# Kernel tuning notes

Measured on AMD Instinct MI355X. Metric: run time of the kernel, lower is better.

Reference implementation:

```python
import jax, jax.numpy as jnp
import numpy as np

NUM_CLUSTERS = 64
DIM = 512
ALPHA = 100.0
EPS = 1e-12  # torch F.normalize eps


def setup_inputs() -> dict:
    key = jax.random.key(0)
    k1, k2 = jax.random.split(key)
    x1 = jax.random.normal(k1, (30, DIM, 28, 28), dtype=jnp.float32)
    centroids = jax.random.uniform(k2, (NUM_CLUSTERS, DIM), dtype=jnp.float32)
    # _init_params: conv weight = 2*alpha*centroids (1x1 conv), bias = -alpha*||centroid||
    conv_w = 2.0 * ALPHA * centroids
    conv_b = -ALPHA * jnp.linalg.norm(centroids, axis=1)
    return {"x1": x1, "centroids": centroids, "conv_w": conv_w, "conv_b": conv_b}


def _l2norm(v, axis):
    n = jnp.sqrt(jnp.sum(v * v, axis=axis, keepdims=True))
    return v / jnp.maximum(n, EPS)


def reference(x1, centroids, conv_w, conv_b):
    T, C, H, W = x1.shape
    K, D = centroids.shape
    x = x1.reshape(T, C, H * W)            # [T, C, N]
    x = _l2norm(x, axis=1)                 # normalize_input: L2 over channel dim
    # 1x1 conv == matmul over channels: logits [T, K, N]
    logits = jnp.einsum('kc,tcn->tkn', conv_w, x) + conv_b[None, :, None]
    a = jax.nn.softmax(logits, axis=1)     # soft assignment over clusters
    # vlad[t,k,c] = sum_n a[t,k,n]*(x[t,c,n] - centroids[k,c])
    # rewritten as two small matmuls, avoiding the [K,C,N] residual tensor
    vlad = jnp.einsum('tkn,tcn->tkc', a, x) - a.sum(axis=-1)[:, :, None] * centroids[None]
    vlad = _l2norm(vlad, axis=2)           # intra-normalization over feature dim
    v = vlad.reshape(T, K * D)
    v = _l2norm(v, axis=1)                 # global L2 normalization
    return v.sum(axis=0, keepdims=True)    # [1, K*D] accumulated over 30 timesteps
```

## Files before the change

kernel.cpp:

```cpp
#include <hip/hip_runtime.h>
#include <math.h>

#define T_ 30
#define C_ 512
#define N_ 784
#define NP_ 832
#define EPSV 1e-12f

typedef __attribute__((ext_vector_type(8))) short bf16x8;
typedef __attribute__((ext_vector_type(4))) float f32x4;

__device__ __forceinline__ unsigned short f2bf(float f) {
    union { float f; unsigned int u; } v; v.f = f;
    unsigned int r = (v.u + 0x7FFFu + ((v.u >> 16) & 1u)) >> 16;
    return (unsigned short)r;
}
__device__ __forceinline__ float bf2f(unsigned short h) {
    union { unsigned int u; float f; } v; v.u = ((unsigned int)h) << 16;
    return v.f;
}

__global__ void k_prep(const float* __restrict__ w, unsigned short* __restrict__ wh,
                       unsigned short* __restrict__ wl) {
    int idx = blockIdx.x * 256 + threadIdx.x;
    float v = w[idx];
    unsigned short h = f2bf(v);
    wh[idx] = h;
    wl[idx] = f2bf(v - bf2f(h));
}

__global__ __launch_bounds__(256) void k_assign(
    const float* __restrict__ x, const unsigned short* __restrict__ wh,
    const unsigned short* __restrict__ wl, const float* __restrict__ b,
    unsigned short* __restrict__ aT, float* __restrict__ asum)
{
    __shared__ __align__(16) unsigned short xhT[64 * 130];
    __shared__ __align__(16) unsigned short xlT[64 * 130];
    __shared__ float bloc[64], invl[64], asl[64], ssred[4][64];

    int t = blockIdx.y, n0 = blockIdx.x * 64;
    int tid = threadIdx.x;
    int w = tid >> 6, L = tid & 63, lid = L & 15, quad = L >> 4;

    if (tid < 64) { bloc[tid] = b[tid]; asl[tid] = 0.f; }

    int li = tid & 15;
    int crg = tid >> 4;
    int nbase = n0 + li * 4;
    float ss0 = 0.f, ss1 = 0.f, ss2 = 0.f, ss3 = 0.f;

    f32x4 acc[4];
    #pragma unroll
    for (int mt = 0; mt < 4; ++mt)
        #pragma unroll
        for (int r = 0; r < 4; ++r) acc[mt][r] = 0.f;

    for (int ch = 0; ch < 4; ++ch) {
        int c0 = ch * 128;
        #pragma unroll
        for (int p = 0; p < 8; ++p) {
            int cl = p * 16 + crg;
            const float* xp = x + ((size_t)t * C_ + c0 + cl) * N_ + nbase;
            float v0, v1, v2, v3;
            if (nbase + 3 < N_) {
                float4 q = *reinterpret_cast<const float4*>(xp);
                v0 = q.x; v1 = q.y; v2 = q.z; v3 = q.w;
            } else {
                v0 = (nbase + 0 < N_) ? xp[0] : 0.f;
                v1 = (nbase + 1 < N_) ? xp[1] : 0.f;
                v2 = (nbase + 2 < N_) ? xp[2] : 0.f;
                v3 = (nbase + 3 < N_) ? xp[3] : 0.f;
            }
            ss0 = fmaf(v0, v0, ss0); ss1 = fmaf(v1, v1, ss1);
            ss2 = fmaf(v2, v2, ss2); ss3 = fmaf(v3, v3, ss3);
            float vv[4] = {v0, v1, v2, v3};
            #pragma unroll
            for (int j = 0; j < 4; ++j) {
                unsigned short h = f2bf(vv[j]);
                xhT[(li * 4 + j) * 130 + cl] = h;
                xlT[(li * 4 + j) * 130 + cl] = f2bf(vv[j] - bf2f(h));
            }
        }
        __syncthreads();
        #pragma unroll
        for (int ks = 0; ks < 4; ++ks) {
            int cl = ks * 32 + quad * 8;
            bf16x8 bh = *reinterpret_cast<const bf16x8*>(&xhT[(w * 16 + lid) * 130 + cl]);
            bf16x8 blo = *reinterpret_cast<const bf16x8*>(&xlT[(w * 16 + lid) * 130 + cl]);
            int cg = c0 + cl;
            #pragma unroll
            for (int mt = 0; mt < 4; ++mt) {
                bf16x8 ah = *reinterpret_cast<const bf16x8*>(wh + (mt * 16 + lid) * 512 + cg);
                bf16x8 al = *reinterpret_cast<const bf16x8*>(wl + (mt * 16 + lid) * 512 + cg);
                acc[mt] = __builtin_amdgcn_mfma_f32_16x16x32_bf16(ah, bh, acc[mt], 0, 0, 0);
                acc[mt] = __builtin_amdgcn_mfma_f32_16x16x32_bf16(ah, blo, acc[mt], 0, 0, 0);
                acc[mt] = __builtin_amdgcn_mfma_f32_16x16x32_bf16(al, bh, acc[mt], 0, 0, 0);
            }
        }
        __syncthreads();
    }

    ss0 += __shfl_xor(ss0, 16, 64); ss0 += __shfl_xor(ss0, 32, 64);
    ss1 += __shfl_xor(ss1, 16, 64); ss1 += __shfl_xor(ss1, 32, 64);
    ss2 += __shfl_xor(ss2, 16, 64); ss2 += __shfl_xor(ss2, 32, 64);
    ss3 += __shfl_xor(ss3, 16, 64); ss3 += __shfl_xor(ss3, 32, 64);
    if (quad == 0) {
        ssred[w][li * 4 + 0] = ss0; ssred[w][li * 4 + 1] = ss1;
        ssred[w][li * 4 + 2] = ss2; ssred[w][li * 4 + 3] = ss3;
    }
    __syncthreads();
    if (tid < 64) {
        float s = ssred[0][tid] + ssred[1][tid] + ssred[2][tid] + ssred[3][tid];
        invl[tid] = 1.0f / fmaxf(sqrtf(s), EPSV);
    }
    __syncthreads();

    int n_lane = n0 + w * 16 + lid;
    bool valid = n_lane < N_;
    float inv = valid ? invl[w * 16 + lid] : 0.f;
    float lg[16];
    float mx = -1e30f;
    #pragma unroll
    for (int mt = 0; mt < 4; ++mt)
        #pragma unroll
        for (int r = 0; r < 4; ++r) {
            float v = fmaf(acc[mt][r], inv, bloc[mt * 16 + quad * 4 + r]);
            lg[mt * 4 + r] = v;
            mx = fmaxf(mx, v);
        }
    mx = fmaxf(mx, __shfl_xor(mx, 16, 64));
    mx = fmaxf(mx, __shfl_xor(mx, 32, 64));
    float se = 0.f;
    #pragma unroll
    for (int u = 0; u < 16; ++u) { lg[u] = __expf(lg[u] - mx); se += lg[u]; }
    se += __shfl_xor(se, 16, 64);
    se += __shfl_xor(se, 32, 64);
    float rs = 1.0f / se;

    size_t base = (size_t)t * 64 * NP_ + n_lane;
    #pragma unroll
    for (int mt = 0; mt < 4; ++mt)
        #pragma unroll
        for (int r = 0; r < 4; ++r) {
            int k = mt * 16 + quad * 4 + r;
            float a = lg[mt * 4 + r] * rs;
            aT[base + (size_t)k * NP_] = valid ? f2bf(a * inv) : (unsigned short)0;
            float ak = valid ? a : 0.f;
            ak += __shfl_xor(ak, 1, 64); ak += __shfl_xor(ak, 2, 64);
            ak += __shfl_xor(ak, 4, 64); ak += __shfl_xor(ak, 8, 64);
            if (lid == 0) atomicAdd(&asl[k], ak);
        }
    __syncthreads();
    if (tid < 64) atomicAdd(&asum[t * 64 + tid], asl[tid]);
}

__global__ __launch_bounds__(256) void k_vlad(
    const float* __restrict__ x, const unsigned short* __restrict__ aT,
    const float* __restrict__ asum, const float* __restrict__ cent,
    float* __restrict__ vlad)
{
    int t = blockIdx.y, cb = blockIdx.x;
    int tid = threadIdx.x;
    int w = tid >> 6, L = tid & 63, lid = L & 15, quad = L >> 4;
    int c = cb * 64 + w * 16 + lid;

    f32x4 acc[4];
    #pragma unroll
    for (int mt = 0; mt < 4; ++mt)
        #pragma unroll
        for (int r = 0; r < 4; ++r) acc[mt][r] = 0.f;

    const float* xrow = x + ((size_t)t * C_ + c) * N_;
    const unsigned short* ab = aT + (size_t)t * 64 * NP_;

    for (int s = 0; s < 25; ++s) {
        int nb0 = s * 32;
        int nb = nb0 + quad * 8;
        if (nb > N_ - 8) nb = N_ - 8;
        float4 x0 = *reinterpret_cast<const float4*>(xrow + nb);
        float4 x1 = *reinterpret_cast<const float4*>(xrow + nb + 4);
        bf16x8 bb;
        bb[0] = (short)f2bf(x0.x); bb[1] = (short)f2bf(x0.y);
        bb[2] = (short)f2bf(x0.z); bb[3] = (short)f2bf(x0.w);
        bb[4] = (short)f2bf(x1.x); bb[5] = (short)f2bf(x1.y);
        bb[6] = (short)f2bf(x1.z); bb[7] = (short)f2bf(x1.w);
        #pragma unroll
        for (int mt = 0; mt < 4; ++mt) {
            bf16x8 af = *reinterpret_cast<const bf16x8*>(
                ab + (size_t)(mt * 16 + lid) * NP_ + nb0 + quad * 8);
            acc[mt] = __builtin_amdgcn_mfma_f32_16x16x32_bf16(af, bb, acc[mt], 0, 0, 0);
        }
    }
    #pragma unroll
    for (int mt = 0; mt < 4; ++mt)
        #pragma unroll
        for (int r = 0; r < 4; ++r) {
            int k = mt * 16 + quad * 4 + r;
            float v = acc[mt][r] - asum[t * 64 + k] * cent[k * 512 + c];
            vlad[((size_t)t * 64 + k) * 512 + c] = v;
        }
}

__global__ void k_intra(const float* __restrict__ vlad, float* __restrict__ inv_intra,
                        float* __restrict__ g) {
    int w = blockIdx.x * 4 + (threadIdx.x >> 6);
    int lane = threadIdx.x & 63;
    const float* vp = vlad + (size_t)w * 512 + lane;
    float s = 0.f;
    #pragma unroll
    for (int j = 0; j < 8; ++j) { float v = vp[j * 64]; s = fmaf(v, v, s); }
    #pragma unroll
    for (int m = 32; m >= 1; m >>= 1) s += __shfl_xor(s, m, 64);
    float inv = 1.0f / fmaxf(sqrtf(s), EPSV);
    if (lane == 0) { inv_intra[w] = inv; g[w] = s * inv * inv; }
}

__global__ void k_global(const float* __restrict__ g, float* __restrict__ inv_g) {
    int t = threadIdx.x;
    if (t < T_) {
        float s = 0.f;
        for (int k = 0; k < 64; ++k) s += g[t * 64 + k];
        inv_g[t] = 1.0f / fmaxf(sqrtf(s), EPSV);
    }
}

__global__ void k_out(const float* __restrict__ vlad, const float* __restrict__ inv_intra,
                      const float* __restrict__ inv_g, float* __restrict__ out) {
    int idx = blockIdx.x * 256 + threadIdx.x;
    int k = idx >> 9;
    float s = 0.f;
    #pragma unroll 5
    for (int t = 0; t < T_; ++t)
        s += vlad[(size_t)t * 32768 + idx] * inv_intra[t * 64 + k] * inv_g[t];
    out[idx] = s;
}

extern "C" void kernel_launch(void* const* d_in, const int* in_sizes, int n_in,
                              void* d_out, int out_size, void* d_ws, size_t ws_size,
                              hipStream_t stream) {
    const float* x    = (const float*)d_in[0];
    const float* cent = (const float*)d_in[1];
    const float* w    = (const float*)d_in[2];
    const float* b    = (const float*)d_in[3];
    float* out = (float*)d_out;

    float* ws = (float*)d_ws;
    unsigned short* wh = (unsigned short*)ws;
    unsigned short* wl = wh + 32768;
    float* asum = (float*)(wl + 32768);
    unsigned short* aT = (unsigned short*)(asum + 1920);
    float* vlad = (float*)(aT + (size_t)T_ * 64 * NP_);
    float* inv_intra = vlad + 983040;
    float* g         = inv_intra + 1920;
    float* inv_g     = g + 1920;

    k_prep<<<128, 256, 0, stream>>>(w, wh, wl);
    hipMemsetAsync(asum, 0, 1920 * sizeof(float), stream);
    k_assign<<<dim3(13, T_), 256, 0, stream>>>(x, wh, wl, b, aT, asum);
    k_vlad<<<dim3(8, T_), 256, 0, stream>>>(x, aT, asum, cent, vlad);
    k_intra<<<480, 256, 0, stream>>>(vlad, inv_intra, g);
    k_global<<<1, 64, 0, stream>>>(g, inv_g);
    k_out<<<128, 256, 0, stream>>>(vlad, inv_intra, inv_g, out);
}
```

Measured before the change: 161.1 us.

## Add transpose/precast pass and split assign/vlad into single-wave blocks

Adds a k_trans kernel that reads x once, computes per-pixel sum of squares via atomics, and writes bf16 hi/lo copies in [n,c] layout plus a bf16 [c,n] copy for the vlad stage. k_assign and k_vlad then run as 64-thread single-wave blocks over many more blocks, reading the pre-cast bf16 data directly instead of converting fp32 inside through LDS. k_global is folded into k_out. The aim is better parallelism and less conversion work. The cost is an extra pass writing about three bf16 copies of x and extra memsets.

After: 176.8 us. 9.8% more time.

```diff
diff --git a/kernel.cpp b/kernel.cpp
--- a/kernel.cpp
+++ b/kernel.cpp
@@ -5,6 +5,7 @@
 #define C_ 512
 #define N_ 784
 #define NP_ 832
+#define NB_ 800
 #define EPSV 1e-12f
 
 typedef __attribute__((ext_vector_type(8))) short bf16x8;
@@ -29,25 +30,86 @@
     wl[idx] = f2bf(v - bf2f(h));
 }
 
-__global__ __launch_bounds__(256) void k_assign(
-    const float* __restrict__ x, const unsigned short* __restrict__ wh,
-    const unsigned short* __restrict__ wl, const float* __restrict__ b,
+__global__ __launch_bounds__(256) void k_trans(
+    const float* __restrict__ x, unsigned short* __restrict__ xh,
+    unsigned short* __restrict__ xl, unsigned short* __restrict__ xcn,
+    float* __restrict__ sumsq)
+{
+    __shared__ float sx[64][65];
+    __shared__ float wred[4][64];
+    int nt = blockIdx.x, ct = blockIdx.y, t = blockIdx.z;
+    int n0 = nt * 64, c0 = ct * 64;
+    int tid = threadIdx.x;
+    int cr = tid >> 4, li = tid & 15;
+    int w = tid >> 6;
+    float ss[4] = {0.f, 0.f, 0.f, 0.f};
+
+    #pragma unroll
+    for (int j = 0; j < 4; ++j) {
+        int cl = j * 16 + cr;
+        int n = n0 + li * 4;
+        float4 q = make_float4(0.f, 0.f, 0.f, 0.f);
+        if (n < N_)
+            q = *reinterpret_cast<const float4*>(x + ((size_t)t * C_ + c0 + cl) * N_ + n);
+        ss[0] = fmaf(q.x, q.x, ss[0]); ss[1] = fmaf(q.y, q.y, ss[1]);
+        ss[2] = fmaf(q.z, q.z, ss[2]); ss[3] = fmaf(q.w, q.w, ss[3]);
+        sx[cl][li * 4 + 0] = q.x; sx[cl][li * 4 + 1] = q.y;
+        sx[cl][li * 4 + 2] = q.z; sx[cl][li * 4 + 3] = q.w;
+    }
+    #pragma unroll
+    for (int i = 0; i < 4; ++i) {
+        ss[i] += __shfl_xor(ss[i], 16, 64);
+        ss[i] += __shfl_xor(ss[i], 32, 64);
+    }
+    if (((tid >> 4) & 3) == 0) {
+        wred[w][li * 4 + 0] = ss[0]; wred[w][li * 4 + 1] = ss[1];
+        wred[w][li * 4 + 2] = ss[2]; wred[w][li * 4 + 3] = ss[3];
+    }
+    __syncthreads();
+    if (tid < 64 && n0 + tid < N_) {
+        float s = wred[0][tid] + wred[1][tid] + wred[2][tid] + wred[3][tid];
+        atomicAdd(&sumsq[t * N_ + n0 + tid], s);
+    }
+    {
+        int li2 = tid & 15, nr = tid >> 4;
+        #pragma unroll
+        for (int j = 0; j < 4; ++j) {
+            int nl = nr + j * 16;
+            ushort4 h, l;
+            float v0 = sx[li2 * 4 + 0][nl], v1 = sx[li2 * 4 + 1][nl];
+            float v2 = sx[li2 * 4 + 2][nl], v3 = sx[li2 * 4 + 3][nl];
+            h.x = f2bf(v0); l.x = f2bf(v0 - bf2f(h.x));
+            h.y = f2bf(v1); l.y = f2bf(v1 - bf2f(h.y));
+            h.z = f2bf(v2); l.z = f2bf(v2 - bf2f(h.z));
+            h.w = f2bf(v3); l.w = f2bf(v3 - bf2f(h.w));
+            size_t o = ((size_t)t * NP_ + n0 + nl) * C_ + c0 + li2 * 4;
+            *reinterpret_cast<ushort4*>(xh + o) = h;
+            *reinterpret_cast<ushort4*>(xl + o) = l;
+        }
+    }
+    #pragma unroll
+    for (int j = 0; j < 4; ++j) {
+        int cl = j * 16 + cr;
+        int n = n0 + li * 4;
+        if (n < NB_) {
+            ushort4 h;
+            h.x = f2bf(sx[cl][li * 4 + 0]); h.y = f2bf(sx[cl][li * 4 + 1]);
+            h.z = f2bf(sx[cl][li * 4 + 2]); h.w = f2bf(sx[cl][li * 4 + 3]);
+            *reinterpret_cast<ushort4*>(xcn + ((size_t)t * C_ + c0 + cl) * NB_ + n) = h;
+        }
+    }
+}
+
+__global__ __launch_bounds__(64) void k_assign(
+    const unsigned short* __restrict__ xh, const unsigned short* __restrict__ xl,
+    const unsigned short* __restrict__ wh, const unsigned short* __restrict__ wl,
+    const float* __restrict__ b, const float* __restrict__ sumsq,
     unsigned short* __restrict__ aT, float* __restrict__ asum)
 {
-    __shared__ __align__(16) unsigned short xhT[64 * 130];
-    __shared__ __align__(16) unsigned short xlT[64 * 130];
-    __shared__ float bloc[64], invl[64], asl[64], ssred[4][64];
-
-    int t = blockIdx.y, n0 = blockIdx.x * 64;
-    int tid = threadIdx.x;
-    int w = tid >> 6, L = tid & 63, lid = L & 15, quad = L >> 4;
-
-    if (tid < 64) { bloc[tid] = b[tid]; asl[tid] = 0.f; }
-
-    int li = tid & 15;
-    int crg = tid >> 4;
-    int nbase = n0 + li * 4;
-    float ss0 = 0.f, ss1 = 0.f, ss2 = 0.f, ss3 = 0.f;
+    int t = blockIdx.y;
+    int n0 = blockIdx.x * 16;
+    int L = threadIdx.x & 63, lid = L & 15, quad = L >> 4;
+    int n_lane = n0 + lid;
 
     f32x4 acc[4];
     #pragma unroll
@@ -55,76 +117,43 @@
         #pragma unroll
         for (int r = 0; r < 4; ++r) acc[mt][r] = 0.f;
 
-    for (int ch = 0; ch < 4; ++ch) {
-        int c0 = ch * 128;
-        #pragma unroll
-        for (int p = 0; p < 8; ++p) {
-            int cl = p * 16 + crg;
-            const float* xp = x + ((size_t)t * C_ + c0 + cl) * N_ + nbase;
-            float v0, v1, v2, v3;
-            if (nbase + 3 < N_) {
-                float4 q = *reinterpret_cast<const float4*>(xp);
-                v0 = q.x; v1 = q.y; v2 = q.z; v3 = q.w;
-            } else {
-                v0 = (nbase + 0 < N_) ? xp[0] : 0.f;
-                v1 = (nbase + 1 < N_) ? xp[1] : 0.f;
-                v2 = (nbase + 2 < N_) ? xp[2] : 0.f;
-                v3 = (nbase + 3 < N_) ? xp[3] : 0.f;
-            }
-            ss0 = fmaf(v0, v0, ss0); ss1 = fmaf(v1, v1, ss1);
-            ss2 = fmaf(v2, v2, ss2); ss3 = fmaf(v3, v3, ss3);
-            float vv[4] = {v0, v1, v2, v3};
-            #pragma unroll
-            for (int j = 0; j < 4; ++j) {
-                unsigned short h = f2bf(vv[j]);
-                xhT[(li * 4 + j) * 130 + cl] = h;
-                xlT[(li * 4 + j) * 130 + cl] = f2bf(vv[j] - bf2f(h));
-            }
-        }
-        __syncthreads();
-        #pragma unroll
-        for (int ks = 0; ks < 4; ++ks) {
-            int cl = ks * 32 + quad * 8;
-            bf16x8 bh = *reinterpret_cast<const bf16x8*>(&xhT[(w * 16 + lid) * 130 + cl]);
-            bf16x8 blo = *reinterpret_cast<const bf16x8*>(&xlT[(w * 16 + lid) * 130 + cl]);
-            int cg = c0 + cl;
-            #pragma unroll
-            for (int mt = 0; mt < 4; ++mt) {
-                bf16x8 ah = *reinterpret_cast<const bf16x8*>(wh + (mt * 16 + lid) * 512 + cg);
-                bf16x8 al = *reinterpret_cast<const bf16x8*>(wl + (mt * 16 + lid) * 512 + cg);
-                acc[mt] = __builtin_amdgcn_mfma_f32_16x16x32_bf16(ah, bh, acc[mt], 0, 0, 0);
-                acc[mt] = __builtin_amdgcn_mfma_f32_16x16x32_bf16(ah, blo, acc[mt], 0, 0, 0);
-                acc[mt] = __builtin_amdgcn_mfma_f32_16x16x32_bf16(al, bh, acc[mt], 0, 0, 0);
-            }
-        }
-        __syncthreads();
-    }
-
-    ss0 += __shfl_xor(ss0, 16, 64); ss0 += __shfl_xor(ss0, 32, 64);
-    ss1 += __shfl_xor(ss1, 16, 64); ss1 += __shfl_xor(ss1, 32, 64);
-    ss2 += __shfl_xor(ss2, 16, 64); ss2 += __shfl_xor(ss2, 32, 64);
-    ss3 += __shfl_xor(ss3, 16, 64); ss3 += __shfl_xor(ss3, 32, 64);
-    if (quad == 0) {
-        ssred[w][li * 4 + 0] = ss0; ssred[w][li * 4 + 1] = ss1;
-        ssred[w][li * 4 + 2] = ss2; ssred[w][li * 4 + 3] = ss3;
-    }
-    __syncthreads();
-    if (tid < 64) {
-        float s = ssred[0][tid] + ssred[1][tid] + ssred[2][tid] + ssred[3][tid];
-        invl[tid] = 1.0f / fmaxf(sqrtf(s), EPSV);
-    }
-    __syncthreads();
-
-    int n_lane = n0 + w * 16 + lid;
+    const unsigned short* bp = xh + ((size_t)t * NP_ + n_lane) * C_ + quad * 8;
+    const unsigned short* blp = xl + ((size_t)t * NP_ + n_lane) * C_ + quad * 8;
+
+    #pragma unroll 4
+    for (int ks = 0; ks < 16; ++ks) {
+        int cs = ks * 32;
+        bf16x8 bh = *reinterpret_cast<const bf16x8*>(bp + cs);
+        bf16x8 bl = *reinterpret_cast<const bf16x8*>(blp + cs);
+        #pragma unroll
+        for (int mt = 0; mt < 4; ++mt) {
+            const unsigned short* ar = wh + (size_t)(mt * 16 + lid) * C_ + cs + quad * 8;
+            const unsigned short* alr = wl + (size_t)(mt * 16 + lid) * C_ + cs + quad * 8;
+            bf16x8 ah = *reinterpret_cast<const bf16x8*>(ar);
+            bf16x8 al = *reinterpret_cast<const bf16x8*>(alr);
+            acc[mt] = __builtin_amdgcn_mfma_f32_16x16x32_bf16(ah, bh, acc[mt], 0, 0, 0);
+            acc[mt] = __builtin_amdgcn_mfma_f32_16x16x32_bf16(al, bh, acc[mt], 0, 0, 0);
+            acc[mt] = __builtin_amdgcn_mfma_f32_16x16x32_bf16(ah, bl, acc[mt], 0, 0, 0);
+        }
+    }
+
     bool valid = n_lane < N_;
-    float inv = valid ? invl[w * 16 + lid] : 0.f;
+    float inv = 0.f;
+    if (valid) {
+        float s = sumsq[t * N_ + n_lane];
+        inv = 1.0f / fmaxf(sqrtf(s), EPSV);
+    }
+    f32x4 bv[4];
+    #pragma unroll
+    for (int mt = 0; mt < 4; ++mt)
+        bv[mt] = *reinterpret_cast<const f32x4*>(b + mt * 16 + quad * 4);
     float lg[16];
     float mx = -1e30f;
     #pragma unroll
     for (int mt = 0; mt < 4; ++mt)
         #pragma unroll
         for (int r = 0; r < 4; ++r) {
-            float v = fmaf(acc[mt][r], inv, bloc[mt * 16 + quad * 4 + r]);
+            float v = fmaf(acc[mt][r], inv, bv[mt][r]);
             lg[mt * 4 + r] = v;
             mx = fmaxf(mx, v);
         }
@@ -137,32 +166,29 @@
     se += __shfl_xor(se, 32, 64);
     float rs = 1.0f / se;
 
-    size_t base = (size_t)t * 64 * NP_ + n_lane;
+    size_t abase = (size_t)t * 64 * NP_ + n_lane;
     #pragma unroll
     for (int mt = 0; mt < 4; ++mt)
         #pragma unroll
         for (int r = 0; r < 4; ++r) {
             int k = mt * 16 + quad * 4 + r;
             float a = lg[mt * 4 + r] * rs;
-            aT[base + (size_t)k * NP_] = valid ? f2bf(a * inv) : (unsigned short)0;
+            aT[abase + (size_t)k * NP_] = valid ? f2bf(a * inv) : (unsigned short)0;
             float ak = valid ? a : 0.f;
             ak += __shfl_xor(ak, 1, 64); ak += __shfl_xor(ak, 2, 64);
             ak += __shfl_xor(ak, 4, 64); ak += __shfl_xor(ak, 8, 64);
-            if (lid == 0) atomicAdd(&asl[k], ak);
-        }
-    __syncthreads();
-    if (tid < 64) atomicAdd(&asum[t * 64 + tid], asl[tid]);
-}
-
-__global__ __launch_bounds__(256) void k_vlad(
-    const float* __restrict__ x, const unsigned short* __restrict__ aT,
+            if (lid == 0) atomicAdd(&asum[t * 64 + k], ak);
+        }
+}
+
+__global__ __launch_bounds__(64) void k_vlad(
+    const unsigned short* __restrict__ xcn, const unsigned short* __restrict__ aT,
     const float* __restrict__ asum, const float* __restrict__ cent,
     float* __restrict__ vlad)
 {
-    int t = blockIdx.y, cb = blockIdx.x;
-    int tid = threadIdx.x;
-    int w = tid >> 6, L = tid & 63, lid = L & 15, quad = L >> 4;
-    int c = cb * 64 + w * 16 + lid;
+    int t = blockIdx.y;
+    int L = threadIdx.x & 63, lid = L & 15, quad = L >> 4;
+    int c = blockIdx.x * 16 + lid;
 
     f32x4 acc[4];
     #pragma unroll
@@ -170,24 +196,16 @@
         #pragma unroll
         for (int r = 0; r < 4; ++r) acc[mt][r] = 0.f;
 
-    const float* xrow = x + ((size_t)t * C_ + c) * N_;
-    const unsigned short* ab = aT + (size_t)t * 64 * NP_;
-
+    const unsigned short* xr = xcn + ((size_t)t * C_ + c) * NB_ + quad * 8;
+    const unsigned short* ab = aT + (size_t)t * 64 * NP_ + quad * 8;
+
+    #pragma unroll 5
     for (int s = 0; s < 25; ++s) {
-        int nb0 = s * 32;
-        int nb = nb0 + quad * 8;
-        if (nb > N_ - 8) nb = N_ - 8;
-        float4 x0 = *reinterpret_cast<const float4*>(xrow + nb);
-        float4 x1 = *reinterpret_cast<const float4*>(xrow + nb + 4);
-        bf16x8 bb;
-        bb[0] = (short)f2bf(x0.x); bb[1] = (short)f2bf(x0.y);
-        bb[2] = (short)f2bf(x0.z); bb[3] = (short)f2bf(x0.w);
-        bb[4] = (short)f2bf(x1.x); bb[5] = (short)f2bf(x1.y);
-        bb[6] = (short)f2bf(x1.z); bb[7] = (short)f2bf(x1.w);
+        int nb = s * 32;
+        bf16x8 bb = *reinterpret_cast<const bf16x8*>(xr + nb);
         #pragma unroll
         for (int mt = 0; mt < 4; ++mt) {
-            bf16x8 af = *reinterpret_cast<const bf16x8*>(
-                ab + (size_t)(mt * 16 + lid) * NP_ + nb0 + quad * 8);
+            bf16x8 af = *reinterpret_cast<const bf16x8*>(ab + (size_t)(mt * 16 + lid) * NP_ + nb);
             acc[mt] = __builtin_amdgcn_mfma_f32_16x16x32_bf16(af, bb, acc[mt], 0, 0, 0);
         }
     }
@@ -215,23 +233,23 @@
     if (lane == 0) { inv_intra[w] = inv; g[w] = s * inv * inv; }
 }
 
-__global__ void k_global(const float* __restrict__ g, float* __restrict__ inv_g) {
-    int t = threadIdx.x;
-    if (t < T_) {
+__global__ void k_out(const float* __restrict__ vlad, const float* __restrict__ inv_intra,
+                      const float* __restrict__ g, float* __restrict__ out) {
+    __shared__ float sinv[T_];
+    int tid = threadIdx.x;
+    if (tid < T_) {
         float s = 0.f;
-        for (int k = 0; k < 64; ++k) s += g[t * 64 + k];
-        inv_g[t] = 1.0f / fmaxf(sqrtf(s), EPSV);
-    }
-}
-
-__global__ void k_out(const float* __restrict__ vlad, const float* __restrict__ inv_intra,
-                      const float* __restrict__ inv_g, float* __restrict__ out) {
-    int idx = blockIdx.x * 256 + threadIdx.x;
+        #pragma unroll 8
+        for (int k = 0; k < 64; ++k) s += g[tid * 64 + k];
+        sinv[tid] = 1.0f / fmaxf(sqrtf(s), EPSV);
+    }
+    __syncthreads();
+    int idx = blockIdx.x * 256 + tid;
     int k = idx >> 9;
     float s = 0.f;
     #pragma unroll 5
     for (int t = 0; t < T_; ++t)
-        s += vlad[(size_t)t * 32768 + idx] * inv_intra[t * 64 + k] * inv_g[t];
+        s += vlad[(size_t)t * 32768 + idx] * inv_intra[t * 64 + k] * sinv[t];
     out[idx] = s;
 }
 
@@ -244,21 +262,25 @@
     const float* b    = (const float*)d_in[3];
     float* out = (float*)d_out;
 
-    float* ws = (float*)d_ws;
-    unsigned short* wh = (unsigned short*)ws;
-    unsigned short* wl = wh + 32768;
-    float* asum = (float*)(wl + 32768);
-    unsigned short* aT = (unsigned short*)(asum + 1920);
-    float* vlad = (float*)(aT + (size_t)T_ * 64 * NP_);
-    float* inv_intra = vlad + 983040;
-    float* g         = inv_intra + 1920;
-    float* inv_g     = g + 1920;
+    char* p = (char*)d_ws;
+    unsigned short* wh = (unsigned short*)p;  p += 65536;
+    unsigned short* wl = (unsigned short*)p;  p += 65536;
+    float* sumsq = (float*)p;                 p += 30 * 784 * 4;
+    float* asum  = (float*)p;                 p += 1920 * 4;
+    unsigned short* aT = (unsigned short*)p;  p += (size_t)30 * 64 * NP_ * 2;
+    unsigned short* xh = (unsigned short*)p;  p += (size_t)30 * NP_ * C_ * 2;
+    unsigned short* xl = (unsigned short*)p;  p += (size_t)30 * NP_ * C_ * 2;
+    unsigned short* xcn = (unsigned short*)p; p += (size_t)30 * C_ * NB_ * 2;
+    float* vlad = (float*)p;                  p += (size_t)983040 * 4;
+    float* inv_intra = (float*)p;             p += 7680;
+    float* g = (float*)p;                     p += 7680;
 
     k_prep<<<128, 256, 0, stream>>>(w, wh, wl);
-    hipMemsetAsync(asum, 0, 1920 * sizeof(float), stream);
-    k_assign<<<dim3(13, T_), 256, 0, stream>>>(x, wh, wl, b, aT, asum);
-    k_vlad<<<dim3(8, T_), 256, 0, stream>>>(x, aT, asum, cent, vlad);
+    hipMemsetAsync(sumsq, 0, 30 * 784 * 4, stream);
+    hipMemsetAsync(asum, 0, 1920 * 4, stream);
+    k_trans<<<dim3(13, 8, T_), 256, 0, stream>>>(x, xh, xl, xcn, sumsq);
+    k_assign<<<dim3(52, T_), 64, 0, stream>>>(xh, xl, wh, wl, b, sumsq, aT, asum);
+    k_vlad<<<dim3(32, T_), 64, 0, stream>>>(xcn, aT, asum, cent, vlad);
     k_intra<<<480, 256, 0, stream>>>(vlad, inv_intra, g);
-    k_global<<<1, 64, 0, stream>>>(g, inv_g);
-    k_out<<<128, 256, 0, stream>>>(vlad, inv_intra, inv_g, out);
-}
+    k_out<<<128, 256, 0, stream>>>(vlad, inv_intra, g, out);
+}
```

## Split channel reduction across waves, raise grid size, fuse norm kernels

Applied to the files above, without the earlier changes.

k_assign now uses 16-pixel tiles (49x30 blocks) with the channel dimension split across the four waves and reduced through LDS. k_vlad uses 16-channel tiles (32x30 blocks) with the pixel dimension split across waves, and it also accumulates squared norms by atomic adds. This removes the separate k_intra and k_global kernels, which are folded into k_out. The aim is higher occupancy on a GPU with many CUs and fewer launches, at the cost of an extra LDS reduction, more atomics, and an added memset of aT.

New measurement: 150.9 us. -6.4%, faster.

```diff
diff --git a/kernel.cpp b/kernel.cpp
--- a/kernel.cpp
+++ b/kernel.cpp
@@ -4,7 +4,8 @@
 #define T_ 30
 #define C_ 512
 #define N_ 784
-#define NP_ 832
+#define NA_ 800
+#define XPITCH 520
 #define EPSV 1e-12f
 
 typedef __attribute__((ext_vector_type(8))) short bf16x8;
@@ -34,20 +35,49 @@
     const unsigned short* __restrict__ wl, const float* __restrict__ b,
     unsigned short* __restrict__ aT, float* __restrict__ asum)
 {
-    __shared__ __align__(16) unsigned short xhT[64 * 130];
-    __shared__ __align__(16) unsigned short xlT[64 * 130];
-    __shared__ float bloc[64], invl[64], asl[64], ssred[4][64];
-
-    int t = blockIdx.y, n0 = blockIdx.x * 64;
+    __shared__ __align__(16) char smem[2 * 16 * XPITCH * 2];
+    unsigned short* xh = (unsigned short*)smem;
+    unsigned short* xl = xh + 16 * XPITCH;
+    float* red = (float*)smem;
+    __shared__ float ssq[4][16];
+    __shared__ float invl[16];
+
+    int t = blockIdx.y, n0 = blockIdx.x * 16;
     int tid = threadIdx.x;
     int w = tid >> 6, L = tid & 63, lid = L & 15, quad = L >> 4;
 
-    if (tid < 64) { bloc[tid] = b[tid]; asl[tid] = 0.f; }
-
-    int li = tid & 15;
-    int crg = tid >> 4;
-    int nbase = n0 + li * 4;
+    int nseg = (tid & 3) * 4;
+    int crow = tid >> 2;
     float ss0 = 0.f, ss1 = 0.f, ss2 = 0.f, ss3 = 0.f;
+    #pragma unroll
+    for (int p = 0; p < 8; ++p) {
+        int c = p * 64 + crow;
+        float4 q = *reinterpret_cast<const float4*>(
+            x + ((size_t)t * C_ + c) * N_ + n0 + nseg);
+        ss0 = fmaf(q.x, q.x, ss0); ss1 = fmaf(q.y, q.y, ss1);
+        ss2 = fmaf(q.z, q.z, ss2); ss3 = fmaf(q.w, q.w, ss3);
+        float vv[4] = {q.x, q.y, q.z, q.w};
+        #pragma unroll
+        for (int j = 0; j < 4; ++j) {
+            unsigned short h = f2bf(vv[j]);
+            xh[(nseg + j) * XPITCH + c] = h;
+            xl[(nseg + j) * XPITCH + c] = f2bf(vv[j] - bf2f(h));
+        }
+    }
+    #pragma unroll
+    for (int m = 4; m <= 32; m <<= 1) {
+        ss0 += __shfl_xor(ss0, m, 64); ss1 += __shfl_xor(ss1, m, 64);
+        ss2 += __shfl_xor(ss2, m, 64); ss3 += __shfl_xor(ss3, m, 64);
+    }
+    if (L < 4) {
+        ssq[w][L * 4 + 0] = ss0; ssq[w][L * 4 + 1] = ss1;
+        ssq[w][L * 4 + 2] = ss2; ssq[w][L * 4 + 3] = ss3;
+    }
+    __syncthreads();
+    if (tid < 16) {
+        float s = ssq[0][tid] + ssq[1][tid] + ssq[2][tid] + ssq[3][tid];
+        invl[tid] = 1.0f / fmaxf(sqrtf(s), EPSV);
+    }
 
     f32x4 acc[4];
     #pragma unroll
@@ -55,114 +85,64 @@
         #pragma unroll
         for (int r = 0; r < 4; ++r) acc[mt][r] = 0.f;
 
-    for (int ch = 0; ch < 4; ++ch) {
-        int c0 = ch * 128;
-        #pragma unroll
-        for (int p = 0; p < 8; ++p) {
-            int cl = p * 16 + crg;
-            const float* xp = x + ((size_t)t * C_ + c0 + cl) * N_ + nbase;
-            float v0, v1, v2, v3;
-            if (nbase + 3 < N_) {
-                float4 q = *reinterpret_cast<const float4*>(xp);
-                v0 = q.x; v1 = q.y; v2 = q.z; v3 = q.w;
-            } else {
-                v0 = (nbase + 0 < N_) ? xp[0] : 0.f;
-                v1 = (nbase + 1 < N_) ? xp[1] : 0.f;
-                v2 = (nbase + 2 < N_) ? xp[2] : 0.f;
-                v3 = (nbase + 3 < N_) ? xp[3] : 0.f;
-            }
-            ss0 = fmaf(v0, v0, ss0); ss1 = fmaf(v1, v1, ss1);
-            ss2 = fmaf(v2, v2, ss2); ss3 = fmaf(v3, v3, ss3);
-            float vv[4] = {v0, v1, v2, v3};
-            #pragma unroll
-            for (int j = 0; j < 4; ++j) {
-                unsigned short h = f2bf(vv[j]);
-                xhT[(li * 4 + j) * 130 + cl] = h;
-                xlT[(li * 4 + j) * 130 + cl] = f2bf(vv[j] - bf2f(h));
-            }
-        }
-        __syncthreads();
-        #pragma unroll
-        for (int ks = 0; ks < 4; ++ks) {
-            int cl = ks * 32 + quad * 8;
-            bf16x8 bh = *reinterpret_cast<const bf16x8*>(&xhT[(w * 16 + lid) * 130 + cl]);
-            bf16x8 blo = *reinterpret_cast<const bf16x8*>(&xlT[(w * 16 + lid) * 130 + cl]);
-            int cg = c0 + cl;
-            #pragma unroll
-            for (int mt = 0; mt < 4; ++mt) {
-                bf16x8 ah = *reinterpret_cast<const bf16x8*>(wh + (mt * 16 + lid) * 512 + cg);
-                bf16x8 al = *reinterpret_cast<const bf16x8*>(wl + (mt * 16 + lid) * 512 + cg);
-                acc[mt] = __builtin_amdgcn_mfma_f32_16x16x32_bf16(ah, bh, acc[mt], 0, 0, 0);
-                acc[mt] = __builtin_amdgcn_mfma_f32_16x16x32_bf16(ah, blo, acc[mt], 0, 0, 0);
-                acc[mt] = __builtin_amdgcn_mfma_f32_16x16x32_bf16(al, bh, acc[mt], 0, 0, 0);
-            }
-        }
-        __syncthreads();
-    }
-
-    ss0 += __shfl_xor(ss0, 16, 64); ss0 += __shfl_xor(ss0, 32, 64);
-    ss1 += __shfl_xor(ss1, 16, 64); ss1 += __shfl_xor(ss1, 32, 64);
-    ss2 += __shfl_xor(ss2, 16, 64); ss2 += __shfl_xor(ss2, 32, 64);
-    ss3 += __shfl_xor(ss3, 16, 64); ss3 += __shfl_xor(ss3, 32, 64);
-    if (quad == 0) {
-        ssred[w][li * 4 + 0] = ss0; ssred[w][li * 4 + 1] = ss1;
-        ssred[w][li * 4 + 2] = ss2; ssred[w][li * 4 + 3] = ss3;
-    }
-    __syncthreads();
-    if (tid < 64) {
-        float s = ssred[0][tid] + ssred[1][tid] + ssred[2][tid] + ssred[3][tid];
-        invl[tid] = 1.0f / fmaxf(sqrtf(s), EPSV);
-    }
-    __syncthreads();
-
-    int n_lane = n0 + w * 16 + lid;
-    bool valid = n_lane < N_;
-    float inv = valid ? invl[w * 16 + lid] : 0.f;
-    float lg[16];
-    float mx = -1e30f;
-    #pragma unroll
-    for (int mt = 0; mt < 4; ++mt)
-        #pragma unroll
-        for (int r = 0; r < 4; ++r) {
-            float v = fmaf(acc[mt][r], inv, bloc[mt * 16 + quad * 4 + r]);
-            lg[mt * 4 + r] = v;
-            mx = fmaxf(mx, v);
-        }
-    mx = fmaxf(mx, __shfl_xor(mx, 16, 64));
-    mx = fmaxf(mx, __shfl_xor(mx, 32, 64));
-    float se = 0.f;
-    #pragma unroll
-    for (int u = 0; u < 16; ++u) { lg[u] = __expf(lg[u] - mx); se += lg[u]; }
-    se += __shfl_xor(se, 16, 64);
-    se += __shfl_xor(se, 32, 64);
-    float rs = 1.0f / se;
-
-    size_t base = (size_t)t * 64 * NP_ + n_lane;
-    #pragma unroll
-    for (int mt = 0; mt < 4; ++mt)
-        #pragma unroll
-        for (int r = 0; r < 4; ++r) {
-            int k = mt * 16 + quad * 4 + r;
-            float a = lg[mt * 4 + r] * rs;
-            aT[base + (size_t)k * NP_] = valid ? f2bf(a * inv) : (unsigned short)0;
-            float ak = valid ? a : 0.f;
-            ak += __shfl_xor(ak, 1, 64); ak += __shfl_xor(ak, 2, 64);
-            ak += __shfl_xor(ak, 4, 64); ak += __shfl_xor(ak, 8, 64);
-            if (lid == 0) atomicAdd(&asl[k], ak);
-        }
-    __syncthreads();
-    if (tid < 64) atomicAdd(&asum[t * 64 + tid], asl[tid]);
+    #pragma unroll
+    for (int ks = 0; ks < 4; ++ks) {
+        int cs = w * 128 + ks * 32;
+        bf16x8 bh = *reinterpret_cast<const bf16x8*>(&xh[lid * XPITCH + cs + quad * 8]);
+        bf16x8 bl = *reinterpret_cast<const bf16x8*>(&xl[lid * XPITCH + cs + quad * 8]);
+        #pragma unroll
+        for (int mt = 0; mt < 4; ++mt) {
+            bf16x8 ah = *reinterpret_cast<const bf16x8*>(wh + (size_t)(mt * 16 + lid) * C_ + cs + quad * 8);
+            bf16x8 al = *reinterpret_cast<const bf16x8*>(wl + (size_t)(mt * 16 + lid) * C_ + cs + quad * 8);
+            acc[mt] = __builtin_amdgcn_mfma_f32_16x16x32_bf16(ah, bh, acc[mt], 0, 0, 0);
+            acc[mt] = __builtin_amdgcn_mfma_f32_16x16x32_bf16(al, bh, acc[mt], 0, 0, 0);
+            acc[mt] = __builtin_amdgcn_mfma_f32_16x16x32_bf16(ah, bl, acc[mt], 0, 0, 0);
+        }
+    }
+    __syncthreads();
+    {
+        float* rp = red + w * (16 * 68);
+        #pragma unroll
+        for (int mt = 0; mt < 4; ++mt)
+            *reinterpret_cast<f32x4*>(&rp[lid * 68 + mt * 16 + quad * 4]) = acc[mt];
+    }
+    __syncthreads();
+
+    float bk = b[L];
+    float asl = 0.f;
+    unsigned short av[4];
+    #pragma unroll
+    for (int i = 0; i < 4; ++i) {
+        int n = w * 4 + i;
+        float v = red[0 * 1088 + n * 68 + L] + red[1 * 1088 + n * 68 + L]
+                + red[2 * 1088 + n * 68 + L] + red[3 * 1088 + n * 68 + L];
+        float inv = invl[n];
+        v = fmaf(v, inv, bk);
+        float mx = v;
+        #pragma unroll
+        for (int m = 1; m <= 32; m <<= 1) mx = fmaxf(mx, __shfl_xor(mx, m, 64));
+        float e = __expf(v - mx);
+        float se = e;
+        #pragma unroll
+        for (int m = 1; m <= 32; m <<= 1) se += __shfl_xor(se, m, 64);
+        float a = e / se;
+        av[i] = f2bf(a * inv);
+        asl += a;
+    }
+    atomicAdd(&asum[t * 64 + L], asl);
+    ushort4 st; st.x = av[0]; st.y = av[1]; st.z = av[2]; st.w = av[3];
+    *reinterpret_cast<ushort4*>(aT + ((size_t)t * 64 + L) * NA_ + n0 + w * 4) = st;
 }
 
 __global__ __launch_bounds__(256) void k_vlad(
     const float* __restrict__ x, const unsigned short* __restrict__ aT,
     const float* __restrict__ asum, const float* __restrict__ cent,
-    float* __restrict__ vlad)
+    float* __restrict__ vlad, float* __restrict__ g2)
 {
-    int t = blockIdx.y, cb = blockIdx.x;
+    __shared__ float red[4][16 * 68];
+    int t = blockIdx.y, c0 = blockIdx.x * 16;
     int tid = threadIdx.x;
     int w = tid >> 6, L = tid & 63, lid = L & 15, quad = L >> 4;
-    int c = cb * 64 + w * 16 + lid;
 
     f32x4 acc[4];
     #pragma unroll
@@ -170,15 +150,14 @@
         #pragma unroll
         for (int r = 0; r < 4; ++r) acc[mt][r] = 0.f;
 
-    const float* xrow = x + ((size_t)t * C_ + c) * N_;
-    const unsigned short* ab = aT + (size_t)t * 64 * NP_;
-
-    for (int s = 0; s < 25; ++s) {
-        int nb0 = s * 32;
-        int nb = nb0 + quad * 8;
-        if (nb > N_ - 8) nb = N_ - 8;
-        float4 x0 = *reinterpret_cast<const float4*>(xrow + nb);
-        float4 x1 = *reinterpret_cast<const float4*>(xrow + nb + 4);
+    const float* xrow = x + ((size_t)t * C_ + c0 + lid) * N_;
+    const unsigned short* ab = aT + (size_t)t * 64 * NA_;
+
+    for (int s = w; s < 25; s += 4) {
+        int nb = s * 32 + quad * 8;
+        int nbc = nb > 776 ? 776 : nb;
+        float4 x0 = *reinterpret_cast<const float4*>(xrow + nbc);
+        float4 x1 = *reinterpret_cast<const float4*>(xrow + nbc + 4);
         bf16x8 bb;
         bb[0] = (short)f2bf(x0.x); bb[1] = (short)f2bf(x0.y);
         bb[2] = (short)f2bf(x0.z); bb[3] = (short)f2bf(x0.w);
@@ -186,52 +165,68 @@
         bb[6] = (short)f2bf(x1.z); bb[7] = (short)f2bf(x1.w);
         #pragma unroll
         for (int mt = 0; mt < 4; ++mt) {
-            bf16x8 af = *reinterpret_cast<const bf16x8*>(
-                ab + (size_t)(mt * 16 + lid) * NP_ + nb0 + quad * 8);
+            bf16x8 af = *reinterpret_cast<const bf16x8*>(ab + (size_t)(mt * 16 + lid) * NA_ + nb);
             acc[mt] = __builtin_amdgcn_mfma_f32_16x16x32_bf16(af, bb, acc[mt], 0, 0, 0);
         }
     }
-    #pragma unroll
-    for (int mt = 0; mt < 4; ++mt)
-        #pragma unroll
-        for (int r = 0; r < 4; ++r) {
-            int k = mt * 16 + quad * 4 + r;
-            float v = acc[mt][r] - asum[t * 64 + k] * cent[k * 512 + c];
-            vlad[((size_t)t * 64 + k) * 512 + c] = v;
-        }
-}
-
-__global__ void k_intra(const float* __restrict__ vlad, float* __restrict__ inv_intra,
-                        float* __restrict__ g) {
-    int w = blockIdx.x * 4 + (threadIdx.x >> 6);
-    int lane = threadIdx.x & 63;
-    const float* vp = vlad + (size_t)w * 512 + lane;
-    float s = 0.f;
-    #pragma unroll
-    for (int j = 0; j < 8; ++j) { float v = vp[j * 64]; s = fmaf(v, v, s); }
-    #pragma unroll
-    for (int m = 32; m >= 1; m >>= 1) s += __shfl_xor(s, m, 64);
-    float inv = 1.0f / fmaxf(sqrtf(s), EPSV);
-    if (lane == 0) { inv_intra[w] = inv; g[w] = s * inv * inv; }
-}
-
-__global__ void k_global(const float* __restrict__ g, float* __restrict__ inv_g) {
-    int t = threadIdx.x;
-    if (t < T_) {
+    {
+        float* rp = &red[w][0];
+        #pragma unroll
+        for (int mt = 0; mt < 4; ++mt)
+            *reinterpret_cast<f32x4*>(&rp[lid * 68 + mt * 16 + quad * 4]) = acc[mt];
+    }
+    __syncthreads();
+
+    int k = tid >> 2, cs4 = (tid & 3) * 4;
+    float as = asum[t * 64 + k];
+    float4 cv = *reinterpret_cast<const float4*>(cent + k * C_ + c0 + cs4);
+    float4 vout;
+    float s2 = 0.f;
+    #pragma unroll
+    for (int j = 0; j < 4; ++j) {
+        int cc = cs4 + j;
+        float v = red[0][cc * 68 + k] + red[1][cc * 68 + k]
+                + red[2][cc * 68 + k] + red[3][cc * 68 + k];
+        v -= as * ((const float*)&cv)[j];
+        ((float*)&vout)[j] = v;
+        s2 = fmaf(v, v, s2);
+    }
+    *reinterpret_cast<float4*>(vlad + ((size_t)t * 64 + k) * C_ + c0 + cs4) = vout;
+    s2 += __shfl_xor(s2, 1, 64);
+    s2 += __shfl_xor(s2, 2, 64);
+    if ((tid & 3) == 0) atomicAdd(&g2[t * 64 + k], s2);
+}
+
+__global__ __launch_bounds__(256) void k_out(
+    const float* __restrict__ vlad, const float* __restrict__ g2,
+    float* __restrict__ out)
+{
+    __shared__ float intr[1920];
+    __shared__ float gl[1920];
+    __shared__ float sinv[T_];
+    int tid = threadIdx.x;
+    for (int i = tid; i < 1920; i += 256) {
+        float s = g2[i];
+        gl[i] = s;
+        intr[i] = 1.0f / fmaxf(sqrtf(s), EPSV);
+    }
+    __syncthreads();
+    if (tid < T_) {
         float s = 0.f;
-        for (int k = 0; k < 64; ++k) s += g[t * 64 + k];
-        inv_g[t] = 1.0f / fmaxf(sqrtf(s), EPSV);
-    }
-}
-
-__global__ void k_out(const float* __restrict__ vlad, const float* __restrict__ inv_intra,
-                      const float* __restrict__ inv_g, float* __restrict__ out) {
-    int idx = blockIdx.x * 256 + threadIdx.x;
+        #pragma unroll 8
+        for (int k = 0; k < 64; ++k) {
+            float iv = intr[tid * 64 + k];
+            s += gl[tid * 64 + k] * iv * iv;
+        }
+        sinv[tid] = 1.0f / fmaxf(sqrtf(s), EPSV);
+    }
+    __syncthreads();
+    int idx = blockIdx.x * 256 + tid;
     int k = idx >> 9;
     float s = 0.f;
     #pragma unroll 5
     for (int t = 0; t < T_; ++t)
-        s += vlad[(size_t)t * 32768 + idx] * inv_intra[t * 64 + k] * inv_g[t];
+        s += vlad[(size_t)t * 32768 + idx] * intr[t * 64 + k] * sinv[t];
     out[idx] = s;
 }
 
@@ -244,21 +239,18 @@
     const float* b    = (const float*)d_in[3];
     float* out = (float*)d_out;
 
-    float* ws = (float*)d_ws;
-    unsigned short* wh = (unsigned short*)ws;
-    unsigned short* wl = wh + 32768;
-    float* asum = (float*)(wl + 32768);
-    unsigned short* aT = (unsigned short*)(asum + 1920);
-    float* vlad = (float*)(aT + (size_t)T_ * 64 * NP_);
-    float* inv_intra = vlad + 983040;
-    float* g         = inv_intra + 1920;
-    float* inv_g     = g + 1920;
+    char* p = (char*)d_ws;
+    unsigned short* wh = (unsigned short*)p;  p += 65536;
+    unsigned short* wl = (unsigned short*)p;  p += 65536;
+    float* asum = (float*)p;                  p += 1920 * 4;
+    float* g2   = (float*)p;                  p += 1920 * 4;
+    unsigned short* aT = (unsigned short*)p;  p += (size_t)T_ * 64 * NA_ * 2;
+    float* vlad = (float*)p;                  p += (size_t)T_ * 64 * C_ * 4;
 
     k_prep<<<128, 256, 0, stream>>>(w, wh, wl);
-    hipMemsetAsync(asum, 0, 1920 * sizeof(float), stream);
-    k_assign<<<dim3(13, T_), 256, 0, stream>>>(x, wh, wl, b, aT, asum);
-    k_vlad<<<dim3(8, T_), 256, 0, stream>>>(x, aT, asum, cent, vlad);
-    k_intra<<<480, 256, 0, stream>>>(vlad, inv_intra, g);
-    k_global<<<1, 64, 0, stream>>>(g, inv_g);
-    k_out<<<128, 256, 0, stream>>>(vlad, inv_intra, inv_g, out);
-}
+    hipMemsetAsync(asum, 0, 2 * 1920 * 4, stream);
+    hipMemsetAsync(aT, 0, (size_t)T_ * 64 * NA_ * 2, stream);
+    k_assign<<<dim3(49, T_), 256, 0, stream>>>(x, wh, wl, b, aT, asum);
+    k_vlad<<<dim3(32, T_), 256, 0, stream>>>(x, aT, asum, cent, vlad, g2);
+    k_out<<<128, 256, 0, stream>>>(vlad, g2, out);
+}
```
